# Kernel tuning notes

Hardware: AMD Instinct MI355X
Metric: run time of the kernel (lower is better)

## Reference

```python
import jax, jax.numpy as jnp
import numpy as np

N_NODES = 8      # objects per graph (fixed in source)
N_AT = 16        # anchors/targets vocab: 8 colors + 8 markers
H = 128          # n_hidden
BS = 16384


def _mlp(x, W1, b1, W2, b2):
    # layers.fully_connected default activation is relu; second layer linear.
    # dropout is identity in eval mode.
    return jax.nn.relu(x @ W1 + b1) @ W2 + b2


def _edges_and_segments(bs):
    # static edge list: all ordered pairs (i,j), i != j, per graph, offset per batch
    ii, jj = np.meshgrid(np.arange(N_NODES), np.arange(N_NODES), indexing='ij')
    m = ii != jj
    base = np.stack([ii[m], jj[m]], axis=1)                      # [56, 2]
    offs = (np.arange(bs) * N_NODES)[:, None, None]
    edges = (base[None] + offs).reshape(-1, 2).astype(np.int32)  # [bs*56, 2]
    seg_ids = np.repeat(np.arange(bs), N_NODES).astype(np.int32) # [bs*8]
    return jnp.asarray(edges), jnp.asarray(seg_ids)


def setup_inputs() -> dict:
    key = jax.random.key(0)
    ks = jax.random.split(key, 14)

    anchors = jax.random.randint(ks[0], (BS,), 0, N_AT)
    n_jumps = jax.random.randint(ks[1], (BS,), 0, N_NODES)
    positions = jax.random.uniform(ks[2], (BS, N_NODES, 2), dtype=jnp.float32)
    colors = jax.random.randint(ks[3], (BS, N_NODES), 0, 8)
    markers = jax.random.randint(ks[4], (BS, N_NODES), 8, 16)  # markers live in [8,16)

    def lin(k, fan_in, fan_out):
        return jax.random.normal(k, (fan_in, fan_out), dtype=jnp.float32) / np.sqrt(fan_in)

    d_in = 2 + 8 + 8 + N_AT + N_NODES  # pos + color_oh + marker_oh + question(16+8) = 42
    z = lambda n: jnp.zeros((n,), jnp.float32)
    return {
        'anchors': anchors, 'n_jumps': n_jumps, 'positions': positions,
        'colors': colors, 'markers': markers,
        'pre_W1': lin(ks[5], d_in, H),     'pre_b1': z(H),
        'pre_W2': lin(ks[6], H, H),        'pre_b2': z(H),
        'msg_W1': lin(ks[7], 2 * H + 1, H),'msg_b1': z(H),
        'msg_W2': lin(ks[8], H, H),        'msg_b2': z(H),
        'post_W1': lin(ks[9], 2 * H, H),   'post_b1': z(H),
        'post_W2': lin(ks[10], H, H),      'post_b2': z(H),
        'out_W1': lin(ks[11], H, H),       'out_b1': z(H),
        'out_W2': lin(ks[12], H, N_AT),    'out_b2': z(N_AT),
    }


def reference(anchors, n_jumps, positions, colors, markers,
              pre_W1, pre_b1, pre_W2, pre_b2,
              msg_W1, msg_b1, msg_W2, msg_b2,
              post_W1, post_b1, post_W2, post_b2,
              out_W1, out_b1, out_W2, out_b2):
    bs = positions.shape[0]
    edges, seg_ids = _edges_and_segments(bs)
    n_total = bs * N_NODES

    col_oh = jax.nn.one_hot(colors, 8, dtype=jnp.float32).reshape(n_total, 8)
    mrk_oh = jax.nn.one_hot(markers - 8, 8, dtype=jnp.float32).reshape(n_total, 8)
    pos = positions.reshape(n_total, 2)

    # pairwise euclidean distance per edge -> [E, 1]
    dp = pos[edges[:, 0]] - pos[edges[:, 1]]
    dist = jnp.sqrt(jnp.sum(dp * dp, axis=1, keepdims=True))

    # question broadcast to every node of its graph
    q = jnp.concatenate([jax.nn.one_hot(anchors, N_AT, dtype=jnp.float32),
                         jax.nn.one_hot(n_jumps, N_NODES, dtype=jnp.float32)], axis=1)
    q = q[seg_ids]  # [bs*8, 24]

    x0 = _mlp(jnp.concatenate([pos, col_oh, mrk_oh, q], axis=1),
              pre_W1, pre_b1, pre_W2, pre_b2)  # [bs*8, H]

    # one message-passing step: gather -> MLP -> scatter(segment_sum on source idx)
    mi = jnp.concatenate([x0[edges[:, 0]], x0[edges[:, 1]], dist], axis=1)  # [E, 257]
    msgs = _mlp(mi, msg_W1, msg_b1, msg_W2, msg_b2)                          # [E, H]
    upd = jax.ops.segment_sum(msgs, edges[:, 0], num_segments=n_total)       # [bs*8, H]

    x = _mlp(jnp.concatenate([upd, x0], axis=1), post_W1, post_b1, post_W2, post_b2)

    logits = jax.ops.segment_sum(x, seg_ids, num_segments=bs)  # [bs, H]
    logits = _mlp(logits, out_W1, out_b1, out_W2, out_b2)      # [bs, 16]
    return logits
```

## Files before the change

### kernel.cpp

```cpp
#include <hip/hip_runtime.h>

#define LROW 136
#define FSTR 72

typedef __bf16 bf16x8  __attribute__((ext_vector_type(8)));
typedef __bf16 bf16x2v __attribute__((ext_vector_type(2)));
typedef float  f32x4   __attribute__((ext_vector_type(4)));
typedef float  f32x2   __attribute__((ext_vector_type(2)));

#define MFMA16(a, b, c) __builtin_amdgcn_mfma_f32_16x16x32_bf16((a), (b), (c), 0, 0, 0)

__device__ __forceinline__ float bflo(unsigned v) { return __uint_as_float(v << 16); }
__device__ __forceinline__ float bfhi(unsigned v) { return __uint_as_float(v & 0xffff0000u); }

__device__ __forceinline__ unsigned short f2bf_u16(float f) {
  unsigned u = __float_as_uint(f);
  u += 0x7fffu + ((u >> 16) & 1u);
  return (unsigned short)(u >> 16);
}

__global__ void combine_weights(
    const float* __restrict__ pre_W1, const float* __restrict__ pre_b1,
    const float* __restrict__ pre_W2, const float* __restrict__ msg_W1,
    const float* __restrict__ msg_W2, const float* __restrict__ post_W1,
    const float* __restrict__ post_W2, const float* __restrict__ out_W1,
    const float* __restrict__ out_W2, const float* __restrict__ pre_b2,
    const float* __restrict__ msg_b1, const float* __restrict__ msg_b2,
    const float* __restrict__ post_b1, const float* __restrict__ post_b2,
    const float* __restrict__ out_b1,
    unsigned short* __restrict__ WabT, unsigned short* __restrict__ WdT,
    unsigned short* __restrict__ WcT, unsigned short* __restrict__ WoT,
    unsigned short* __restrict__ Wo2T, unsigned short* __restrict__ W1pT,
    float* __restrict__ vecs)
{
  __shared__ float part[256];
  const int b = blockIdx.x;
  const int t = threadIdx.x;
  if (b < 320) {
    const int p  = b >> 6;
    const int kp = b & 63;
    const int k  = kp * 2 + (t >> 7);
    const int n  = t & 127;
    const float* L; const float* R; unsigned short* O;
    if (p == 0)      { L = pre_W2;  R = msg_W1;             O = WabT; }
    else if (p == 1) { L = pre_W2;  R = msg_W1 + 128*128;   O = WabT + 128*128; }
    else if (p == 2) { L = pre_W2;  R = post_W1 + 128*128;  O = WdT; }
    else if (p == 3) { L = msg_W2;  R = post_W1;            O = WcT; }
    else             { L = post_W2; R = out_W1;             O = WoT; }
    const float* Lr = L + k * 128;
    float a0 = 0.f, a1 = 0.f, a2 = 0.f, a3 = 0.f;
    #pragma unroll 8
    for (int m = 0; m < 128; m += 4) {
      a0 = fmaf(Lr[m + 0], R[(m + 0) * 128 + n], a0);
      a1 = fmaf(Lr[m + 1], R[(m + 1) * 128 + n], a1);
      a2 = fmaf(Lr[m + 2], R[(m + 2) * 128 + n], a2);
      a3 = fmaf(Lr[m + 3], R[(m + 3) * 128 + n], a3);
    }
    O[n * 128 + k] = f2bf_u16((a0 + a1) + (a2 + a3));
  } else if (b == 320) {
    for (int idx = t; idx < 16 * 128; idx += 256) {
      int o = idx >> 7, k = idx & 127;
      Wo2T[o * 128 + k] = f2bf_u16(out_W2[k * 16 + o]);
    }
    if (t < 128) vecs[t] = msg_W1[256 * 128 + t];
    for (int idx = t; idx < 128 * 64; idx += 256) {
      int n = idx >> 6, k = idx & 63;
      float v = (k < 42) ? pre_W1[k * 128 + n] : (k == 42 ? pre_b1[n] : 0.f);
      W1pT[n * 64 + k] = f2bf_u16(v);
    }
  } else {
    const int n = t & 127;
    const int h = t >> 7;
    float s = 0.f;
    if (b == 321) {
      #pragma unroll 8
      for (int m = h * 64; m < h * 64 + 64; ++m)
        s = fmaf(pre_b2[m], msg_W1[m * 128 + n] + msg_W1[(128 + m) * 128 + n], s);
    } else if (b == 322) {
      #pragma unroll 8
      for (int m = h * 64; m < h * 64 + 64; ++m) {
        s = fmaf(7.f * msg_b2[m], post_W1[m * 128 + n], s);
        s = fmaf(pre_b2[m], post_W1[(128 + m) * 128 + n], s);
      }
    } else {
      #pragma unroll 8
      for (int m = h * 64; m < h * 64 + 64; ++m)
        s = fmaf(8.f * post_b2[m], out_W1[m * 128 + n], s);
    }
    part[t] = s;
    __syncthreads();
    if (t < 128) {
      float r = part[t] + part[t + 128];
      if (b == 321)      vecs[128 + t] = r + msg_b1[t];
      else if (b == 322) vecs[256 + t] = r + post_b1[t];
      else               vecs[384 + t] = r + out_b1[t];
    }
  }
}

__global__ void __launch_bounds__(256, 4) rrn_main(
    const int* __restrict__ anchors, const int* __restrict__ n_jumps,
    const float* __restrict__ positions, const int* __restrict__ colors,
    const int* __restrict__ markers,
    const __bf16* __restrict__ W1pT,
    const __bf16* __restrict__ WabT, const __bf16* __restrict__ WdT,
    const __bf16* __restrict__ WcT, const __bf16* __restrict__ WoT,
    const __bf16* __restrict__ Wo2T, const float* __restrict__ vecs,
    const float* __restrict__ out_b2, float* __restrict__ out)
{
  __shared__ __align__(16) char smem[38912];
  __bf16* featL = (__bf16*)(smem);
  __bf16* Ab    = (__bf16*)(smem);
  __bf16* h1    = (__bf16*)(smem + 17408);
  __bf16* Bb    = (__bf16*)(smem + 17408);
  __bf16* Sph   = (__bf16*)(smem + 17408);
  __bf16* hob   = (__bf16*)(smem + 21760);
  float*  dist  = (float*)(smem + 34816);
  float*  vec   = (float*)(smem + 36864);

  const int tid  = threadIdx.x;
  const int lane = tid & 63;
  const int w    = tid >> 6;
  const int l15  = lane & 15;
  const int quad = lane >> 4;
  const int colw = w * 32;
  const int crow = colw + 2 * l15;
  const int g0   = blockIdx.x * 8;
  const int n0   = blockIdx.x * 64;

  if (tid < 64) {
    uint4* rp = (uint4*)&featL[tid * FSTR];
    uint4 z4 = {0u, 0u, 0u, 0u};
    #pragma unroll
    for (int i = 0; i < 9; ++i) rp[i] = z4;
    int g = tid >> 3;
    float px = positions[(n0 + tid) * 2], py = positions[(n0 + tid) * 2 + 1];
    int c  = colors[n0 + tid], mk = markers[n0 + tid] - 8;
    int a  = anchors[g0 + g],  nj = n_jumps[g0 + g];
    __bf16* row = &featL[tid * FSTR];
    row[0] = (__bf16)px; row[1] = (__bf16)py;
    const __bf16 one = (__bf16)1.f;
    row[2 + c] = one; row[10 + mk] = one;
    row[18 + a] = one; row[34 + nj] = one;
    row[42] = one;
  }
  for (int i = tid; i < 512; i += 256) {
    int g = i >> 6, ii = (i >> 3) & 7, jj = i & 7;
    const float* pa = positions + (n0 + g * 8 + ii) * 2;
    const float* pb = positions + (n0 + g * 8 + jj) * 2;
    float dx = pa[0] - pb[0], dy = pa[1] - pb[1];
    dist[i] = sqrtf(dx * dx + dy * dy);
  }
  for (int i = tid; i < 512; i += 256) vec[i] = vecs[i];
  __syncthreads();

  {
    f32x4 acch[4][2];
    f32x4 zero = {0.f, 0.f, 0.f, 0.f};
    #pragma unroll
    for (int mt = 0; mt < 4; ++mt) { acch[mt][0] = zero; acch[mt][1] = zero; }
    #pragma unroll
    for (int kb = 0; kb < 64; kb += 32) {
      const int ko = kb + quad * 8;
      bf16x8 fa[4], fb[2];
      #pragma unroll
      for (int mt = 0; mt < 4; ++mt)
        fa[mt] = *(const bf16x8*)&featL[(mt * 16 + l15) * FSTR + ko];
      fb[0] = *(const bf16x8*)&W1pT[(crow) * 64 + ko];
      fb[1] = *(const bf16x8*)&W1pT[(crow + 1) * 64 + ko];
      #pragma unroll
      for (int mt = 0; mt < 4; ++mt) {
        acch[mt][0] = MFMA16(fa[mt], fb[0], acch[mt][0]);
        acch[mt][1] = MFMA16(fa[mt], fb[1], acch[mt][1]);
      }
    }
    #pragma unroll
    for (int mt = 0; mt < 4; ++mt)
      #pragma unroll
      for (int r = 0; r < 4; ++r) {
        bf16x2v o = { (__bf16)fmaxf(acch[mt][0][r], 0.f),
                      (__bf16)fmaxf(acch[mt][1][r], 0.f) };
        *(bf16x2v*)&h1[(mt * 16 + quad * 4 + r) * LROW + crow] = o;
      }
  }
  __syncthreads();

  f32x4 acc1[4][4];
  {
    f32x4 zero = {0.f, 0.f, 0.f, 0.f};
    #pragma unroll
    for (int mt = 0; mt < 4; ++mt)
      #pragma unroll
      for (int nt = 0; nt < 4; ++nt) acc1[mt][nt] = zero;
  }
  #pragma unroll
  for (int kb = 0; kb < 128; kb += 32) {
    const int ko = kb + quad * 8;
    bf16x8 fa[4], fb[4];
    #pragma unroll
    for (int mt = 0; mt < 4; ++mt)
      fa[mt] = *(const bf16x8*)&h1[(mt * 16 + l15) * LROW + ko];
    fb[0] = *(const bf16x8*)&WabT[(crow) * 128 + ko];
    fb[1] = *(const bf16x8*)&WabT[(crow + 1) * 128 + ko];
    fb[2] = *(const bf16x8*)&WabT[(128 + crow) * 128 + ko];
    fb[3] = *(const bf16x8*)&WabT[(128 + crow + 1) * 128 + ko];
    #pragma unroll
    for (int mt = 0; mt < 4; ++mt)
      #pragma unroll
      for (int nt = 0; nt < 4; ++nt)
        acc1[mt][nt] = MFMA16(fa[mt], fb[nt], acc1[mt][nt]);
  }
  #pragma unroll
  for (int mt = 0; mt < 4; ++mt)
    #pragma unroll
    for (int r = 0; r < 4; ++r) {
      bf16x2v o = { (__bf16)acc1[mt][0][r], (__bf16)acc1[mt][1][r] };
      *(bf16x2v*)&Ab[(mt * 16 + quad * 4 + r) * LROW + crow] = o;
    }

  f32x4 accD[4][2];
  {
    f32x4 zero = {0.f, 0.f, 0.f, 0.f};
    #pragma unroll
    for (int mt = 0; mt < 4; ++mt) { accD[mt][0] = zero; accD[mt][1] = zero; }
  }
  #pragma unroll
  for (int kb = 0; kb < 128; kb += 32) {
    const int ko = kb + quad * 8;
    bf16x8 fa[4], fd[2];
    #pragma unroll
    for (int mt = 0; mt < 4; ++mt)
      fa[mt] = *(const bf16x8*)&h1[(mt * 16 + l15) * LROW + ko];
    fd[0] = *(const bf16x8*)&WdT[(crow) * 128 + ko];
    fd[1] = *(const bf16x8*)&WdT[(crow + 1) * 128 + ko];
    #pragma unroll
    for (int mt = 0; mt < 4; ++mt) {
      accD[mt][0] = MFMA16(fa[mt], fd[0], accD[mt][0]);
      accD[mt][1] = MFMA16(fa[mt], fd[1], accD[mt][1]);
    }
  }
  __syncthreads();
  #pragma unroll
  for (int mt = 0; mt < 4; ++mt)
    #pragma unroll
    for (int r = 0; r < 4; ++r) {
      bf16x2v o = { (__bf16)acc1[mt][2][r], (__bf16)acc1[mt][3][r] };
      *(bf16x2v*)&Bb[(mt * 16 + quad * 4 + r) * LROW + crow] = o;
    }

  {
    const int c0 = colw + ((l15 & 8) << 1) + 2 * (l15 & 7);
    const f32x2 wv = { vec[c0], vec[c0 + 1] };
    const f32x2 cv = { vec[128 + c0], vec[128 + c0 + 1] };
    const f32x2 z2 = {0.f, 0.f};
    #pragma unroll
    for (int gi = 0; gi < 2; ++gi) {
      const int g = 2 * quad + gi;
      f32x2 Bj[8];
      #pragma unroll
      for (int j = 0; j < 8; ++j) {
        unsigned vb = *(const unsigned*)&Bb[(g * 8 + j) * LROW + c0];
        Bj[j].x = bflo(vb); Bj[j].y = bfhi(vb);
      }
      #pragma unroll
      for (int i = 0; i < 8; ++i) {
        unsigned va = *(const unsigned*)&Ab[(g * 8 + i) * LROW + c0];
        f32x2 a = {bflo(va) + cv.x, bfhi(va) + cv.y};
        f32x2 s = z2;
        #pragma unroll
        for (int j = 0; j < 8; ++j) {
          if (j == i) continue;
          float d = dist[g * 64 + i * 8 + j];
          f32x2 d2 = {d, d};
          f32x2 t = __builtin_elementwise_fma(d2, wv, Bj[j]) + a;
          s += __builtin_elementwise_max(t, z2);
        }
        unsigned o = (unsigned)f2bf_u16(s.x) | ((unsigned)f2bf_u16(s.y) << 16);
        *(unsigned*)&Ab[(g * 8 + i) * LROW + c0] = o;
      }
    }
  }
  __syncthreads();

  {
    const __bf16* Sb = Ab;
    #pragma unroll
    for (int kb = 0; kb < 128; kb += 32) {
      const int ko = kb + quad * 8;
      bf16x8 fa[4], fc[2];
      #pragma unroll
      for (int mt = 0; mt < 4; ++mt)
        fa[mt] = *(const bf16x8*)&Sb[(mt * 16 + l15) * LROW + ko];
      fc[0] = *(const bf16x8*)&WcT[(crow) * 128 + ko];
      fc[1] = *(const bf16x8*)&WcT[(crow + 1) * 128 + ko];
      #pragma unroll
      for (int mt = 0; mt < 4; ++mt) {
        accD[mt][0] = MFMA16(fa[mt], fc[0], accD[mt][0]);
        accD[mt][1] = MFMA16(fa[mt], fc[1], accD[mt][1]);
      }
    }
    const f32x2 cpv = *(const f32x2*)&vec[256 + crow];
    #pragma unroll
    for (int mt = 0; mt < 4; ++mt) {
      f32x4 a0 = accD[mt][0];
      f32x4 a1 = accD[mt][1];
      float s0 = fmaxf(a0[0] + cpv.x, 0.f) + fmaxf(a0[1] + cpv.x, 0.f)
               + fmaxf(a0[2] + cpv.x, 0.f) + fmaxf(a0[3] + cpv.x, 0.f);
      float s1 = fmaxf(a1[0] + cpv.y, 0.f) + fmaxf(a1[1] + cpv.y, 0.f)
               + fmaxf(a1[2] + cpv.y, 0.f) + fmaxf(a1[3] + cpv.y, 0.f);
      s0 += __shfl_xor(s0, 16);
      s1 += __shfl_xor(s1, 16);
      int grow = mt * 2 + (lane >= 32 ? 1 : 0);
      if ((lane & 31) < 16) {
        bf16x2v o = { (__bf16)s0, (__bf16)s1 };
        *(bf16x2v*)&Sph[grow * LROW + crow] = o;
      } else {
        *(unsigned*)&Sph[(8 + grow) * LROW + crow] = 0u;
      }
    }
  }
  __syncthreads();

  {
    f32x4 acco[2];
    f32x4 zero = {0.f, 0.f, 0.f, 0.f};
    acco[0] = zero; acco[1] = zero;
    #pragma unroll
    for (int kb = 0; kb < 128; kb += 32) {
      const int ko = kb + quad * 8;
      bf16x8 fa = *(const bf16x8*)&Sph[l15 * LROW + ko];
      bf16x8 fb0 = *(const bf16x8*)&WoT[(crow) * 128 + ko];
      bf16x8 fb1 = *(const bf16x8*)&WoT[(crow + 1) * 128 + ko];
      acco[0] = MFMA16(fa, fb0, acco[0]);
      acco[1] = MFMA16(fa, fb1, acco[1]);
    }
    const f32x2 cov = *(const f32x2*)&vec[384 + crow];
    #pragma unroll
    for (int r = 0; r < 4; ++r) {
      bf16x2v o = { (__bf16)fmaxf(acco[0][r] + cov.x, 0.f),
                    (__bf16)fmaxf(acco[1][r] + cov.y, 0.f) };
      *(bf16x2v*)&hob[(quad * 4 + r) * LROW + crow] = o;
    }
  }
  __syncthreads();

  if (w == 0) {
    f32x4 accf = {0.f, 0.f, 0.f, 0.f};
    #pragma unroll
    for (int kb = 0; kb < 128; kb += 32) {
      const int ko = kb + quad * 8;
      bf16x8 fa  = *(const bf16x8*)&hob[l15 * LROW + ko];
      bf16x8 fbv = *(const bf16x8*)&Wo2T[l15 * 128 + ko];
      accf = MFMA16(fa, fbv, accf);
    }
    if (quad < 2) {
      float b2 = out_b2[l15];
      #pragma unroll
      for (int r = 0; r < 4; ++r) {
        int row = quad * 4 + r;
        out[(g0 + row) * 16 + l15] = accf[r] + b2;
      }
    }
  }
}

extern "C" void kernel_launch(void* const* d_in, const int* in_sizes, int n_in,
                              void* d_out, int out_size, void* d_ws, size_t ws_size,
                              hipStream_t stream) {
  const int*   anchors   = (const int*)d_in[0];
  const int*   n_jumps   = (const int*)d_in[1];
  const float* positions = (const float*)d_in[2];
  const int*   colors    = (const int*)d_in[3];
  const int*   markers   = (const int*)d_in[4];
  const float* pre_W1  = (const float*)d_in[5];
  const float* pre_b1  = (const float*)d_in[6];
  const float* pre_W2  = (const float*)d_in[7];
  const float* pre_b2  = (const float*)d_in[8];
  const float* msg_W1  = (const float*)d_in[9];
  const float* msg_b1  = (const float*)d_in[10];
  const float* msg_W2  = (const float*)d_in[11];
  const float* msg_b2  = (const float*)d_in[12];
  const float* post_W1 = (const float*)d_in[13];
  const float* post_b1 = (const float*)d_in[14];
  const float* post_W2 = (const float*)d_in[15];
  const float* post_b2 = (const float*)d_in[16];
  const float* out_W1  = (const float*)d_in[17];
  const float* out_b1  = (const float*)d_in[18];
  const float* out_W2  = (const float*)d_in[19];
  const float* out_b2  = (const float*)d_in[20];

  char* ws = (char*)d_ws;
  unsigned short* WabT = (unsigned short*)(ws);
  unsigned short* WdT  = (unsigned short*)(ws + 65536);
  unsigned short* WcT  = (unsigned short*)(ws + 98304);
  unsigned short* WoT  = (unsigned short*)(ws + 131072);
  unsigned short* Wo2T = (unsigned short*)(ws + 163840);
  float*          vecs = (float*)(ws + 167936);
  unsigned short* W1pT = (unsigned short*)(ws + 169984);

  const int BS = in_sizes[0];

  combine_weights<<<324, 256, 0, stream>>>(
      pre_W1, pre_b1, pre_W2, msg_W1, msg_W2, post_W1, post_W2, out_W1, out_W2,
      pre_b2, msg_b1, msg_b2, post_b1, post_b2, out_b1,
      WabT, WdT, WcT, WoT, Wo2T, W1pT, vecs);

  rrn_main<<<BS / 8, 256, 0, stream>>>(
      anchors, n_jumps, positions, colors, markers,
      (const __bf16*)W1pT,
      (const __bf16*)WabT, (const __bf16*)WdT, (const __bf16*)WcT,
      (const __bf16*)WoT, (const __bf16*)Wo2T, vecs, out_b2, (float*)d_out);
}
```

Measured before the change: 152.2 us.

## Halve graphs per block to shrink LDS and registers for higher occupancy

Each block now processes 4 graphs (32 nodes) instead of 8, so there are twice as many blocks, shared memory per block is roughly halved, and accumulator register arrays are halved. Launch bounds are raised to allow 5 blocks per CU. The A/B/D GEMM phase is restructured so the B and D accumulations run in one fused loop over the K dimension. In exchange, each block reloads the full weight matrices for half as much work, which doubles weight traffic from L2 and halves MFMA reuse of each loaded weight fragment.

```diff
diff --git a/kernel.cpp b/kernel.cpp
--- a/kernel.cpp
+++ b/kernel.cpp
@@ -98,7 +98,7 @@
   }
 }
 
-__global__ void __launch_bounds__(256, 4) rrn_main(
+__global__ void __launch_bounds__(256, 5) rrn_main(
     const int* __restrict__ anchors, const int* __restrict__ n_jumps,
     const float* __restrict__ positions, const int* __restrict__ colors,
     const int* __restrict__ markers,
@@ -108,15 +108,15 @@
     const __bf16* __restrict__ Wo2T, const float* __restrict__ vecs,
     const float* __restrict__ out_b2, float* __restrict__ out)
 {
-  __shared__ __align__(16) char smem[38912];
+  __shared__ __align__(16) char smem[20480];
   __bf16* featL = (__bf16*)(smem);
   __bf16* Ab    = (__bf16*)(smem);
-  __bf16* h1    = (__bf16*)(smem + 17408);
-  __bf16* Bb    = (__bf16*)(smem + 17408);
-  __bf16* Sph   = (__bf16*)(smem + 17408);
-  __bf16* hob   = (__bf16*)(smem + 21760);
-  float*  dist  = (float*)(smem + 34816);
-  float*  vec   = (float*)(smem + 36864);
+  __bf16* h1    = (__bf16*)(smem + 8704);
+  __bf16* Bb    = (__bf16*)(smem + 8704);
+  __bf16* Sph   = (__bf16*)(smem + 8704);
+  __bf16* hob   = (__bf16*)(smem + 13056);
+  float*  dist  = (float*)(smem + 17408);
+  float*  vec   = (float*)(smem + 18432);
 
   const int tid  = threadIdx.x;
   const int lane = tid & 63;
@@ -125,10 +125,10 @@
   const int quad = lane >> 4;
   const int colw = w * 32;
   const int crow = colw + 2 * l15;
-  const int g0   = blockIdx.x * 8;
-  const int n0   = blockIdx.x * 64;
-
-  if (tid < 64) {
+  const int g0   = blockIdx.x * 4;
+  const int n0   = blockIdx.x * 32;
+
+  if (tid < 32) {
     uint4* rp = (uint4*)&featL[tid * FSTR];
     uint4 z4 = {0u, 0u, 0u, 0u};
     #pragma unroll
@@ -144,7 +144,8 @@
     row[18 + a] = one; row[34 + nj] = one;
     row[42] = one;
   }
-  for (int i = tid; i < 512; i += 256) {
+  {
+    int i = tid;
     int g = i >> 6, ii = (i >> 3) & 7, jj = i & 7;
     const float* pa = positions + (n0 + g * 8 + ii) * 2;
     const float* pb = positions + (n0 + g * 8 + jj) * 2;
@@ -155,27 +156,25 @@
   __syncthreads();
 
   {
-    f32x4 acch[4][2];
+    f32x4 acch[2][2];
     f32x4 zero = {0.f, 0.f, 0.f, 0.f};
-    #pragma unroll
-    for (int mt = 0; mt < 4; ++mt) { acch[mt][0] = zero; acch[mt][1] = zero; }
+    acch[0][0] = zero; acch[0][1] = zero; acch[1][0] = zero; acch[1][1] = zero;
     #pragma unroll
     for (int kb = 0; kb < 64; kb += 32) {
       const int ko = kb + quad * 8;
-      bf16x8 fa[4], fb[2];
-      #pragma unroll
-      for (int mt = 0; mt < 4; ++mt)
-        fa[mt] = *(const bf16x8*)&featL[(mt * 16 + l15) * FSTR + ko];
+      bf16x8 fa[2], fb[2];
+      fa[0] = *(const bf16x8*)&featL[(l15) * FSTR + ko];
+      fa[1] = *(const bf16x8*)&featL[(16 + l15) * FSTR + ko];
       fb[0] = *(const bf16x8*)&W1pT[(crow) * 64 + ko];
       fb[1] = *(const bf16x8*)&W1pT[(crow + 1) * 64 + ko];
       #pragma unroll
-      for (int mt = 0; mt < 4; ++mt) {
+      for (int mt = 0; mt < 2; ++mt) {
         acch[mt][0] = MFMA16(fa[mt], fb[0], acch[mt][0]);
         acch[mt][1] = MFMA16(fa[mt], fb[1], acch[mt][1]);
       }
     }
     #pragma unroll
-    for (int mt = 0; mt < 4; ++mt)
+    for (int mt = 0; mt < 2; ++mt)
       #pragma unroll
       for (int r = 0; r < 4; ++r) {
         bf16x2v o = { (__bf16)fmaxf(acch[mt][0][r], 0.f),
@@ -185,123 +184,119 @@
   }
   __syncthreads();
 
-  f32x4 acc1[4][4];
-  {
+  {
+    f32x4 accA[2][2];
     f32x4 zero = {0.f, 0.f, 0.f, 0.f};
-    #pragma unroll
-    for (int mt = 0; mt < 4; ++mt)
-      #pragma unroll
-      for (int nt = 0; nt < 4; ++nt) acc1[mt][nt] = zero;
-  }
-  #pragma unroll
-  for (int kb = 0; kb < 128; kb += 32) {
-    const int ko = kb + quad * 8;
-    bf16x8 fa[4], fb[4];
-    #pragma unroll
-    for (int mt = 0; mt < 4; ++mt)
-      fa[mt] = *(const bf16x8*)&h1[(mt * 16 + l15) * LROW + ko];
-    fb[0] = *(const bf16x8*)&WabT[(crow) * 128 + ko];
-    fb[1] = *(const bf16x8*)&WabT[(crow + 1) * 128 + ko];
-    fb[2] = *(const bf16x8*)&WabT[(128 + crow) * 128 + ko];
-    fb[3] = *(const bf16x8*)&WabT[(128 + crow + 1) * 128 + ko];
-    #pragma unroll
-    for (int mt = 0; mt < 4; ++mt)
-      #pragma unroll
-      for (int nt = 0; nt < 4; ++nt)
-        acc1[mt][nt] = MFMA16(fa[mt], fb[nt], acc1[mt][nt]);
-  }
-  #pragma unroll
-  for (int mt = 0; mt < 4; ++mt)
-    #pragma unroll
-    for (int r = 0; r < 4; ++r) {
-      bf16x2v o = { (__bf16)acc1[mt][0][r], (__bf16)acc1[mt][1][r] };
-      *(bf16x2v*)&Ab[(mt * 16 + quad * 4 + r) * LROW + crow] = o;
-    }
-
-  f32x4 accD[4][2];
-  {
+    accA[0][0] = zero; accA[0][1] = zero; accA[1][0] = zero; accA[1][1] = zero;
+    #pragma unroll
+    for (int kb = 0; kb < 128; kb += 32) {
+      const int ko = kb + quad * 8;
+      bf16x8 fa[2], fb[2];
+      fa[0] = *(const bf16x8*)&h1[(l15) * LROW + ko];
+      fa[1] = *(const bf16x8*)&h1[(16 + l15) * LROW + ko];
+      fb[0] = *(const bf16x8*)&WabT[(crow) * 128 + ko];
+      fb[1] = *(const bf16x8*)&WabT[(crow + 1) * 128 + ko];
+      accA[0][0] = MFMA16(fa[0], fb[0], accA[0][0]);
+      accA[0][1] = MFMA16(fa[0], fb[1], accA[0][1]);
+      accA[1][0] = MFMA16(fa[1], fb[0], accA[1][0]);
+      accA[1][1] = MFMA16(fa[1], fb[1], accA[1][1]);
+    }
+    #pragma unroll
+    for (int mt = 0; mt < 2; ++mt)
+      #pragma unroll
+      for (int r = 0; r < 4; ++r) {
+        bf16x2v o = { (__bf16)accA[mt][0][r], (__bf16)accA[mt][1][r] };
+        *(bf16x2v*)&Ab[(mt * 16 + quad * 4 + r) * LROW + crow] = o;
+      }
+  }
+
+  f32x4 accD[2][2];
+  {
+    f32x4 accB[2][2];
     f32x4 zero = {0.f, 0.f, 0.f, 0.f};
-    #pragma unroll
-    for (int mt = 0; mt < 4; ++mt) { accD[mt][0] = zero; accD[mt][1] = zero; }
-  }
-  #pragma unroll
-  for (int kb = 0; kb < 128; kb += 32) {
-    const int ko = kb + quad * 8;
-    bf16x8 fa[4], fd[2];
-    #pragma unroll
-    for (int mt = 0; mt < 4; ++mt)
-      fa[mt] = *(const bf16x8*)&h1[(mt * 16 + l15) * LROW + ko];
-    fd[0] = *(const bf16x8*)&WdT[(crow) * 128 + ko];
-    fd[1] = *(const bf16x8*)&WdT[(crow + 1) * 128 + ko];
-    #pragma unroll
-    for (int mt = 0; mt < 4; ++mt) {
-      accD[mt][0] = MFMA16(fa[mt], fd[0], accD[mt][0]);
-      accD[mt][1] = MFMA16(fa[mt], fd[1], accD[mt][1]);
-    }
-  }
-  __syncthreads();
-  #pragma unroll
-  for (int mt = 0; mt < 4; ++mt)
-    #pragma unroll
-    for (int r = 0; r < 4; ++r) {
-      bf16x2v o = { (__bf16)acc1[mt][2][r], (__bf16)acc1[mt][3][r] };
-      *(bf16x2v*)&Bb[(mt * 16 + quad * 4 + r) * LROW + crow] = o;
-    }
+    accB[0][0] = zero; accB[0][1] = zero; accB[1][0] = zero; accB[1][1] = zero;
+    accD[0][0] = zero; accD[0][1] = zero; accD[1][0] = zero; accD[1][1] = zero;
+    #pragma unroll
+    for (int kb = 0; kb < 128; kb += 32) {
+      const int ko = kb + quad * 8;
+      bf16x8 fa[2], fb[2], fd[2];
+      fa[0] = *(const bf16x8*)&h1[(l15) * LROW + ko];
+      fa[1] = *(const bf16x8*)&h1[(16 + l15) * LROW + ko];
+      fb[0] = *(const bf16x8*)&WabT[(128 + crow) * 128 + ko];
+      fb[1] = *(const bf16x8*)&WabT[(128 + crow + 1) * 128 + ko];
+      fd[0] = *(const bf16x8*)&WdT[(crow) * 128 + ko];
+      fd[1] = *(const bf16x8*)&WdT[(crow + 1) * 128 + ko];
+      accB[0][0] = MFMA16(fa[0], fb[0], accB[0][0]);
+      accB[0][1] = MFMA16(fa[0], fb[1], accB[0][1]);
+      accB[1][0] = MFMA16(fa[1], fb[0], accB[1][0]);
+      accB[1][1] = MFMA16(fa[1], fb[1], accB[1][1]);
+      accD[0][0] = MFMA16(fa[0], fd[0], accD[0][0]);
+      accD[0][1] = MFMA16(fa[0], fd[1], accD[0][1]);
+      accD[1][0] = MFMA16(fa[1], fd[0], accD[1][0]);
+      accD[1][1] = MFMA16(fa[1], fd[1], accD[1][1]);
+    }
+    __syncthreads();
+    #pragma unroll
+    for (int mt = 0; mt < 2; ++mt)
+      #pragma unroll
+      for (int r = 0; r < 4; ++r) {
+        bf16x2v o = { (__bf16)accB[mt][0][r], (__bf16)accB[mt][1][r] };
+        *(bf16x2v*)&Bb[(mt * 16 + quad * 4 + r) * LROW + crow] = o;
+      }
+  }
 
   {
     const int c0 = colw + ((l15 & 8) << 1) + 2 * (l15 & 7);
     const f32x2 wv = { vec[c0], vec[c0 + 1] };
     const f32x2 cv = { vec[128 + c0], vec[128 + c0 + 1] };
     const f32x2 z2 = {0.f, 0.f};
-    #pragma unroll
-    for (int gi = 0; gi < 2; ++gi) {
-      const int g = 2 * quad + gi;
-      f32x2 Bj[8];
+    const int g = quad;
+    f32x2 Bj[8];
+    #pragma unroll
+    for (int j = 0; j < 8; ++j) {
+      unsigned vb = *(const unsigned*)&Bb[(g * 8 + j) * LROW + c0];
+      Bj[j].x = bflo(vb); Bj[j].y = bfhi(vb);
+    }
+    #pragma unroll
+    for (int i = 0; i < 8; ++i) {
+      unsigned va = *(const unsigned*)&Ab[(g * 8 + i) * LROW + c0];
+      f32x2 a = {bflo(va) + cv.x, bfhi(va) + cv.y};
+      f32x2 s = z2;
       #pragma unroll
       for (int j = 0; j < 8; ++j) {
-        unsigned vb = *(const unsigned*)&Bb[(g * 8 + j) * LROW + c0];
-        Bj[j].x = bflo(vb); Bj[j].y = bfhi(vb);
-      }
-      #pragma unroll
-      for (int i = 0; i < 8; ++i) {
-        unsigned va = *(const unsigned*)&Ab[(g * 8 + i) * LROW + c0];
-        f32x2 a = {bflo(va) + cv.x, bfhi(va) + cv.y};
-        f32x2 s = z2;
-        #pragma unroll
-        for (int j = 0; j < 8; ++j) {
-          if (j == i) continue;
-          float d = dist[g * 64 + i * 8 + j];
-          f32x2 d2 = {d, d};
-          f32x2 t = __builtin_elementwise_fma(d2, wv, Bj[j]) + a;
-          s += __builtin_elementwise_max(t, z2);
-        }
-        unsigned o = (unsigned)f2bf_u16(s.x) | ((unsigned)f2bf_u16(s.y) << 16);
-        *(unsigned*)&Ab[(g * 8 + i) * LROW + c0] = o;
-      }
+        if (j == i) continue;
+        float d = dist[g * 64 + i * 8 + j];
+        f32x2 d2 = {d, d};
+        f32x2 t = __builtin_elementwise_fma(d2, wv, Bj[j]) + a;
+        s += __builtin_elementwise_max(t, z2);
+      }
+      unsigned o = (unsigned)f2bf_u16(s.x) | ((unsigned)f2bf_u16(s.y) << 16);
+      *(unsigned*)&Ab[(g * 8 + i) * LROW + c0] = o;
     }
   }
   __syncthreads();
 
   {
+    #pragma unroll
+    for (int rr = 0; rr < 3; ++rr)
+      *(unsigned*)&Sph[(4 + quad * 3 + rr) * LROW + crow] = 0u;
     const __bf16* Sb = Ab;
     #pragma unroll
     for (int kb = 0; kb < 128; kb += 32) {
       const int ko = kb + quad * 8;
-      bf16x8 fa[4], fc[2];
-      #pragma unroll
-      for (int mt = 0; mt < 4; ++mt)
-        fa[mt] = *(const bf16x8*)&Sb[(mt * 16 + l15) * LROW + ko];
+      bf16x8 fa[2], fc[2];
+      fa[0] = *(const bf16x8*)&Sb[(l15) * LROW + ko];
+      fa[1] = *(const bf16x8*)&Sb[(16 + l15) * LROW + ko];
       fc[0] = *(const bf16x8*)&WcT[(crow) * 128 + ko];
       fc[1] = *(const bf16x8*)&WcT[(crow + 1) * 128 + ko];
-      #pragma unroll
-      for (int mt = 0; mt < 4; ++mt) {
-        accD[mt][0] = MFMA16(fa[mt], fc[0], accD[mt][0]);
-        accD[mt][1] = MFMA16(fa[mt], fc[1], accD[mt][1]);
-      }
+      accD[0][0] = MFMA16(fa[0], fc[0], accD[0][0]);
+      accD[0][1] = MFMA16(fa[0], fc[1], accD[0][1]);
+      accD[1][0] = MFMA16(fa[1], fc[0], accD[1][0]);
+      accD[1][1] = MFMA16(fa[1], fc[1], accD[1][1]);
     }
     const f32x2 cpv = *(const f32x2*)&vec[256 + crow];
     #pragma unroll
-    for (int mt = 0; mt < 4; ++mt) {
+    for (int mt = 0; mt < 2; ++mt) {
       f32x4 a0 = accD[mt][0];
       f32x4 a1 = accD[mt][1];
       float s0 = fmaxf(a0[0] + cpv.x, 0.f) + fmaxf(a0[1] + cpv.x, 0.f)
@@ -314,8 +309,6 @@
       if ((lane & 31) < 16) {
         bf16x2v o = { (__bf16)s0, (__bf16)s1 };
         *(bf16x2v*)&Sph[grow * LROW + crow] = o;
-      } else {
-        *(unsigned*)&Sph[(8 + grow) * LROW + crow] = 0u;
       }
     }
   }
@@ -353,13 +346,11 @@
       bf16x8 fbv = *(const bf16x8*)&Wo2T[l15 * 128 + ko];
       accf = MFMA16(fa, fbv, accf);
     }
-    if (quad < 2) {
+    if (quad == 0) {
       float b2 = out_b2[l15];
       #pragma unroll
-      for (int r = 0; r < 4; ++r) {
-        int row = quad * 4 + r;
-        out[(g0 + row) * 16 + l15] = accf[r] + b2;
-      }
+      for (int r = 0; r < 4; ++r)
+        out[(g0 + r) * 16 + l15] = accf[r] + b2;
     }
   }
 }
@@ -405,7 +396,7 @@
       pre_b2, msg_b1, msg_b2, post_b1, post_b2, out_b1,
       WabT, WdT, WcT, WoT, Wo2T, W1pT, vecs);
 
-  rrn_main<<<BS / 8, 256, 0, stream>>>(
+  rrn_main<<<BS / 4, 256, 0, stream>>>(
       anchors, n_jumps, positions, colors, markers,
       (const __bf16*)W1pT,
       (const __bf16*)WabT, (const __bf16*)WdT, (const __bf16*)WcT,
```

Result: slower. 189.7 us (+24.6%).

## Compute pairwise edge messages directly from MFMA registers via lane shuffles

Applied to the files above, without the earlier changes.

The A and B projections are no longer staged through shared memory as bf16. The all-pairs message ReLU sum is now computed straight from the MFMA accumulator registers, using xor-16 shuffles to exchange the other half of each graph's neighbour rows. One barrier and two LDS round-trips are removed, the dist array is padded to avoid bank conflicts, and fp32 precision is kept for A and B. In exchange, launch bounds drop to 3 waves per SIMD to allow for the higher register pressure, which may cost occupancy.

```diff
diff --git a/kernel.cpp b/kernel.cpp
--- a/kernel.cpp
+++ b/kernel.cpp
@@ -2,6 +2,7 @@
 
 #define LROW 136
 #define FSTR 72
+#define DSTR 68
 
 typedef __bf16 bf16x8  __attribute__((ext_vector_type(8)));
 typedef __bf16 bf16x2v __attribute__((ext_vector_type(2)));
@@ -98,7 +99,7 @@
   }
 }
 
-__global__ void __launch_bounds__(256, 4) rrn_main(
+__global__ void __launch_bounds__(256, 3) rrn_main(
     const int* __restrict__ anchors, const int* __restrict__ n_jumps,
     const float* __restrict__ positions, const int* __restrict__ colors,
     const int* __restrict__ markers,
@@ -108,15 +109,14 @@
     const __bf16* __restrict__ Wo2T, const float* __restrict__ vecs,
     const float* __restrict__ out_b2, float* __restrict__ out)
 {
-  __shared__ __align__(16) char smem[38912];
+  __shared__ __align__(16) char smem[39040];
   __bf16* featL = (__bf16*)(smem);
-  __bf16* Ab    = (__bf16*)(smem);
+  __bf16* Sb    = (__bf16*)(smem);
   __bf16* h1    = (__bf16*)(smem + 17408);
-  __bf16* Bb    = (__bf16*)(smem + 17408);
   __bf16* Sph   = (__bf16*)(smem + 17408);
   __bf16* hob   = (__bf16*)(smem + 21760);
   float*  dist  = (float*)(smem + 34816);
-  float*  vec   = (float*)(smem + 36864);
+  float*  vec   = (float*)(smem + 36992);
 
   const int tid  = threadIdx.x;
   const int lane = tid & 63;
@@ -149,7 +149,7 @@
     const float* pa = positions + (n0 + g * 8 + ii) * 2;
     const float* pb = positions + (n0 + g * 8 + jj) * 2;
     float dx = pa[0] - pb[0], dy = pa[1] - pb[1];
-    dist[i] = sqrtf(dx * dx + dy * dy);
+    dist[g * DSTR + (i & 63)] = sqrtf(dx * dx + dy * dy);
   }
   for (int i = tid; i < 512; i += 256) vec[i] = vecs[i];
   __syncthreads();
@@ -210,13 +210,6 @@
       for (int nt = 0; nt < 4; ++nt)
         acc1[mt][nt] = MFMA16(fa[mt], fb[nt], acc1[mt][nt]);
   }
-  #pragma unroll
-  for (int mt = 0; mt < 4; ++mt)
-    #pragma unroll
-    for (int r = 0; r < 4; ++r) {
-      bf16x2v o = { (__bf16)acc1[mt][0][r], (__bf16)acc1[mt][1][r] };
-      *(bf16x2v*)&Ab[(mt * 16 + quad * 4 + r) * LROW + crow] = o;
-    }
 
   f32x4 accD[4][2];
   {
@@ -239,51 +232,50 @@
       accD[mt][1] = MFMA16(fa[mt], fd[1], accD[mt][1]);
     }
   }
+
+  {
+    const f32x2 wv = { vec[crow], vec[crow + 1] };
+    const f32x2 cv = { vec[128 + crow], vec[128 + crow + 1] };
+    const int q0 = quad & 1;
+    const int q1 = quad >> 1;
+    const int jo = q0 * 4;
+    const int js = jo ^ 4;
+    #pragma unroll
+    for (int mt = 0; mt < 4; ++mt) {
+      const int g = 2 * mt + q1;
+      float bo0[4], bo1[4], bs0[4], bs1[4];
+      #pragma unroll
+      for (int r = 0; r < 4; ++r) {
+        bo0[r] = acc1[mt][2][r];
+        bo1[r] = acc1[mt][3][r];
+        bs0[r] = __shfl_xor(bo0[r], 16);
+        bs1[r] = __shfl_xor(bo1[r], 16);
+      }
+      const float* dg = &dist[g * DSTR + jo * 8];
+      #pragma unroll
+      for (int rr = 0; rr < 4; ++rr) {
+        const float* di = dg + rr * 8;
+        float a0 = acc1[mt][0][rr] + cv.x;
+        float a1 = acc1[mt][1][rr] + cv.y;
+        float s0 = -fmaxf(a0 + bo0[rr], 0.f);
+        float s1 = -fmaxf(a1 + bo1[rr], 0.f);
+        #pragma unroll
+        for (int r = 0; r < 4; ++r) {
+          float dox = di[jo + r];
+          float dsx = di[js + r];
+          s0 += fmaxf(fmaf(dox, wv.x, bo0[r]) + a0, 0.f);
+          s1 += fmaxf(fmaf(dox, wv.y, bo1[r]) + a1, 0.f);
+          s0 += fmaxf(fmaf(dsx, wv.x, bs0[r]) + a0, 0.f);
+          s1 += fmaxf(fmaf(dsx, wv.y, bs1[r]) + a1, 0.f);
+        }
+        unsigned o = (unsigned)f2bf_u16(s0) | ((unsigned)f2bf_u16(s1) << 16);
+        *(unsigned*)&Sb[(mt * 16 + quad * 4 + rr) * LROW + crow] = o;
+      }
+    }
+  }
   __syncthreads();
-  #pragma unroll
-  for (int mt = 0; mt < 4; ++mt)
-    #pragma unroll
-    for (int r = 0; r < 4; ++r) {
-      bf16x2v o = { (__bf16)acc1[mt][2][r], (__bf16)acc1[mt][3][r] };
-      *(bf16x2v*)&Bb[(mt * 16 + quad * 4 + r) * LROW + crow] = o;
-    }
-
-  {
-    const int c0 = colw + ((l15 & 8) << 1) + 2 * (l15 & 7);
-    const f32x2 wv = { vec[c0], vec[c0 + 1] };
-    const f32x2 cv = { vec[128 + c0], vec[128 + c0 + 1] };
-    const f32x2 z2 = {0.f, 0.f};
-    #pragma unroll
-    for (int gi = 0; gi < 2; ++gi) {
-      const int g = 2 * quad + gi;
-      f32x2 Bj[8];
-      #pragma unroll
-      for (int j = 0; j < 8; ++j) {
-        unsigned vb = *(const unsigned*)&Bb[(g * 8 + j) * LROW + c0];
-        Bj[j].x = bflo(vb); Bj[j].y = bfhi(vb);
-      }
-      #pragma unroll
-      for (int i = 0; i < 8; ++i) {
-        unsigned va = *(const unsigned*)&Ab[(g * 8 + i) * LROW + c0];
-        f32x2 a = {bflo(va) + cv.x, bfhi(va) + cv.y};
-        f32x2 s = z2;
-        #pragma unroll
-        for (int j = 0; j < 8; ++j) {
-          if (j == i) continue;
-          float d = dist[g * 64 + i * 8 + j];
-          f32x2 d2 = {d, d};
-          f32x2 t = __builtin_elementwise_fma(d2, wv, Bj[j]) + a;
-          s += __builtin_elementwise_max(t, z2);
-        }
-        unsigned o = (unsigned)f2bf_u16(s.x) | ((unsigned)f2bf_u16(s.y) << 16);
-        *(unsigned*)&Ab[(g * 8 + i) * LROW + c0] = o;
-      }
-    }
-  }
-  __syncthreads();
-
-  {
-    const __bf16* Sb = Ab;
+
+  {
     #pragma unroll
     for (int kb = 0; kb < 128; kb += 32) {
       const int ko = kb + quad * 8;
```

Measured after the change: 158.0 us. 1.04x slower.
